# Performance work log

Measured on AMD Instinct MI355X. Metric: run time of the kernel, lower is better.

## Reference

```python
import jax, jax.numpy as jnp
import numpy as np

CHI = 24          # bond dimension (A0[0].shape[0])
K_PATHS = 16      # number of sampled spin strings
N_SPINS = 34      # N = 2**k + 2 with k = 5


def setup_inputs() -> dict:
    key = jax.random.key(0)
    k1, k2 = jax.random.split(key)
    # positive entries -> positive traces -> valid probabilities (stochastic MPS regime)
    A = jax.random.uniform(k1, (2, CHI, CHI), dtype=jnp.float32)
    samples = jax.random.randint(k2, (K_PATHS, N_SPINS), 0, 2).astype(jnp.int32)
    return {"A": A, "samples": samples}


def _kron(X, Y):
    d = X.shape[0] * Y.shape[0]
    return jnp.einsum('ij,kl->ikjl', X, Y).reshape(d, d)


def reference(A, samples):
    chi = A.shape[1]
    Au, Ad = A[0], A[1]
    AAu = _kron(Au, Au)              # [chi^2, chi^2]
    AAd = _kron(Ad, Ad)
    E = AAu + AAd                    # transfer matrix
    E2 = E @ E

    N = samples.shape[1]
    log2N = int(np.log2(N - 2))      # static: matches self.log2N
    E2k = E2
    for _ in range(log2N - 1):       # repeated squaring with trace normalization
        E2k = E2k @ E2k
        E2k = E2k / jnp.trace(E2k)
    EN = E2k @ E2                    # E^N up to overall scale

    def path_loglikelihood(spins):
        def step(String, s):
            Su = String @ AAu
            Sd = String @ AAd
            tr_u = jnp.trace(Su)
            tr_d = jnp.trace(Sd)
            tot = tr_u + tr_d
            p = jnp.where(s == 1, tr_u, tr_d) / tot
            # normalize by total trace: probabilities are scale-invariant ratios,
            # so this is mathematically identical but numerically stable
            String_new = jnp.where(s == 1, Su, Sd) / tot
            return String_new, jnp.log(p)

        _, logps = jax.lax.scan(step, EN, spins)
        return jnp.sum(logps)

    ll = jax.vmap(path_loglikelihood)(samples)   # [K_paths]
    return -jnp.sum(ll)                          # negative loglikelihood objective
```

## Files before the change

kernel.cpp:

```cpp
#include <hip/hip_runtime.h>
#include <math.h>


#define CHI      24
#define CHI2     576
#define NPATH    16
#define NSPIN    34
#define NT       512
#define PITERS_R 2
#define PITERS_L 1
#define SCALE_P  0.00390625f
#define SCALE_V  0.0625f

#define LDS_FENCE() asm volatile("s_waitcnt lgkmcnt(0)" ::: "memory")

__device__ __forceinline__ float hsum4(float4 a) { return (a.x + a.z) + (a.y + a.w); }
__device__ __forceinline__ void fma4(float4& acc, const float4 a, const float4 b) {
    acc.x = fmaf(a.x, b.x, acc.x);
    acc.y = fmaf(a.y, b.y, acc.y);
    acc.z = fmaf(a.z, b.z, acc.z);
    acc.w = fmaf(a.w, b.w, acc.w);
}

__device__ __forceinline__ void mm_tile2(const float* __restrict__ Xa,
                                         const float* __restrict__ Xb,
                                         const float* __restrict__ Y,
                                         int i0, int j0, float o1[3][3], float o2[3][3]) {
    const float4* A0 = (const float4*)(Xa + (i0 + 0) * CHI);
    const float4* A1 = (const float4*)(Xa + (i0 + 1) * CHI);
    const float4* A2 = (const float4*)(Xa + (i0 + 2) * CHI);
    const float4* B0 = (const float4*)(Xb + (i0 + 0) * CHI);
    const float4* B1 = (const float4*)(Xb + (i0 + 1) * CHI);
    const float4* B2 = (const float4*)(Xb + (i0 + 2) * CHI);
    const float4* Y0 = (const float4*)(Y + (j0 + 0) * CHI);
    const float4* Y1 = (const float4*)(Y + (j0 + 1) * CHI);
    const float4* Y2 = (const float4*)(Y + (j0 + 2) * CHI);
    float4 p[3][3], q[3][3];
    #pragma unroll
    for (int a = 0; a < 3; ++a)
        #pragma unroll
        for (int b = 0; b < 3; ++b) {
            p[a][b] = make_float4(0.f, 0.f, 0.f, 0.f);
            q[a][b] = make_float4(0.f, 0.f, 0.f, 0.f);
        }
    #pragma unroll
    for (int v = 0; v < 6; ++v) {
        const float4 y0 = Y0[v], y1 = Y1[v], y2 = Y2[v];
        const float4 a0 = A0[v], a1 = A1[v], a2 = A2[v];
        fma4(p[0][0], a0, y0); fma4(p[0][1], a0, y1); fma4(p[0][2], a0, y2);
        fma4(p[1][0], a1, y0); fma4(p[1][1], a1, y1); fma4(p[1][2], a1, y2);
        fma4(p[2][0], a2, y0); fma4(p[2][1], a2, y1); fma4(p[2][2], a2, y2);
        const float4 b0 = B0[v], b1 = B1[v], b2 = B2[v];
        fma4(q[0][0], b0, y0); fma4(q[0][1], b0, y1); fma4(q[0][2], b0, y2);
        fma4(q[1][0], b1, y0); fma4(q[1][1], b1, y1); fma4(q[1][2], b1, y2);
        fma4(q[2][0], b2, y0); fma4(q[2][1], b2, y1); fma4(q[2][2], b2, y2);
    }
    #pragma unroll
    for (int a = 0; a < 3; ++a)
        #pragma unroll
        for (int b = 0; b < 3; ++b) { o1[a][b] = hsum4(p[a][b]); o2[a][b] = hsum4(q[a][b]); }
}

__device__ __forceinline__ void mm_tile_dual(const float* __restrict__ X1,
                                             const float* __restrict__ Y1,
                                             const float* __restrict__ X2,
                                             const float* __restrict__ Y2,
                                             int i0, int j0, float o1[3][3], float o2[3][3]) {
    const float4* A0 = (const float4*)(X1 + (i0 + 0) * CHI);
    const float4* A1 = (const float4*)(X1 + (i0 + 1) * CHI);
    const float4* A2 = (const float4*)(X1 + (i0 + 2) * CHI);
    const float4* U0 = (const float4*)(Y1 + (j0 + 0) * CHI);
    const float4* U1 = (const float4*)(Y1 + (j0 + 1) * CHI);
    const float4* U2 = (const float4*)(Y1 + (j0 + 2) * CHI);
    const float4* B0 = (const float4*)(X2 + (i0 + 0) * CHI);
    const float4* B1 = (const float4*)(X2 + (i0 + 1) * CHI);
    const float4* B2 = (const float4*)(X2 + (i0 + 2) * CHI);
    const float4* V0 = (const float4*)(Y2 + (j0 + 0) * CHI);
    const float4* V1 = (const float4*)(Y2 + (j0 + 1) * CHI);
    const float4* V2 = (const float4*)(Y2 + (j0 + 2) * CHI);
    float4 p[3][3], q[3][3];
    #pragma unroll
    for (int a = 0; a < 3; ++a)
        #pragma unroll
        for (int b = 0; b < 3; ++b) {
            p[a][b] = make_float4(0.f, 0.f, 0.f, 0.f);
            q[a][b] = make_float4(0.f, 0.f, 0.f, 0.f);
        }
    #pragma unroll
    for (int v = 0; v < 6; ++v) {
        const float4 a0 = A0[v], a1 = A1[v], a2 = A2[v];
        const float4 u0 = U0[v], u1 = U1[v], u2 = U2[v];
        fma4(p[0][0], a0, u0); fma4(p[0][1], a0, u1); fma4(p[0][2], a0, u2);
        fma4(p[1][0], a1, u0); fma4(p[1][1], a1, u1); fma4(p[1][2], a1, u2);
        fma4(p[2][0], a2, u0); fma4(p[2][1], a2, u1); fma4(p[2][2], a2, u2);
        const float4 b0 = B0[v], b1 = B1[v], b2 = B2[v];
        const float4 w0 = V0[v], w1 = V1[v], w2 = V2[v];
        fma4(q[0][0], b0, w0); fma4(q[0][1], b0, w1); fma4(q[0][2], b0, w2);
        fma4(q[1][0], b1, w0); fma4(q[1][1], b1, w1); fma4(q[1][2], b1, w2);
        fma4(q[2][0], b2, w0); fma4(q[2][1], b2, w1); fma4(q[2][2], b2, w2);
    }
    #pragma unroll
    for (int a = 0; a < 3; ++a)
        #pragma unroll
        for (int b = 0; b < 3; ++b) { o1[a][b] = hsum4(p[a][b]); o2[a][b] = hsum4(q[a][b]); }
}

__device__ __forceinline__ void st_tile(float* __restrict__ D, int i0, int j0,
                                        const float o[3][3], float s) {
    #pragma unroll
    for (int a = 0; a < 3; ++a)
        #pragma unroll
        for (int b = 0; b < 3; ++b) D[(i0 + a) * CHI + j0 + b] = o[a][b] * s;
}

__device__ __forceinline__ float dot24v(const float4 r[6], const float vb[24]) {
    float a0 = 0.f, a1 = 0.f, a2 = 0.f, a3 = 0.f;
    #pragma unroll
    for (int v = 0; v < 6; ++v) {
        a0 = fmaf(r[v].x, vb[4 * v + 0], a0);
        a1 = fmaf(r[v].y, vb[4 * v + 1], a1);
        a2 = fmaf(r[v].z, vb[4 * v + 2], a2);
        a3 = fmaf(r[v].w, vb[4 * v + 3], a3);
    }
    return (a0 + a2) + (a1 + a3);
}

__global__ __launch_bounds__(NT, 2) void mps_ll_kernel(
    const float* __restrict__ A,
    const int*   __restrict__ samples,
    float*       __restrict__ out)
{
    __shared__ alignas(16) float sAu[CHI2], sAd[CHI2], sAuT[CHI2], sAdT[CHI2];
    __shared__ alignas(16) float sL[CHI2], sR[CHI2], sGu[CHI2], sGd[CHI2];
    __shared__ alignas(16) float bO1[CHI2], bO2[CHI2], bQ1[CHI2], bQ2[CHI2];
    __shared__ alignas(16) float sVH[NSPIN * CHI];
    __shared__ float llw[8];

    const int tid  = threadIdx.x;
    const int w    = tid >> 6;
    const int lane = tid & 63;
    const int path = blockIdx.x;
    const int i0 = 3 * (lane >> 3), j0 = 3 * (lane & 7);

    for (int k = tid; k < CHI2; k += NT) {
        const int r = k / CHI, c = k % CHI;
        const float u = A[k], d = A[CHI2 + k];
        sAu[k] = u; sAd[k] = d;
        sAuT[c * CHI + r] = u; sAdT[c * CHI + r] = d;
        sR[k] = 1.0f; sL[k] = 1.0f;
    }
    const int sp = (lane < NSPIN) ? samples[path * NSPIN + lane] : 0;
    const unsigned long long smask = __ballot(sp != 0);
    __syncthreads();

    if (w == 0) {
        float o1[3][3], o2[3][3];
        for (int it = 0; it <= PITERS_R; ++it) {
            mm_tile2(sAu, sAd, sR, i0, j0, o1, o2);
            LDS_FENCE();
            st_tile(bO1, i0, j0, o1, 1.0f);
            st_tile(bO2, i0, j0, o2, 1.0f);
            LDS_FENCE();
            mm_tile_dual(bO1, sAu, bO2, sAd, i0, j0, o1, o2);
            LDS_FENCE();
            if (it < PITERS_R) {
                #pragma unroll
                for (int a = 0; a < 3; ++a)
                    #pragma unroll
                    for (int b = 0; b < 3; ++b)
                        sR[(i0 + a) * CHI + j0 + b] = (o1[a][b] + o2[a][b]) * SCALE_P;
            } else {
                st_tile(sGu, i0, j0, o1, SCALE_P);
                st_tile(sGd, i0, j0, o2, SCALE_P);
            }
            LDS_FENCE();
        }
    } else {
        int trec0, trec1, tstart;
        if      (w == 1) { trec0 = 0;  trec1 = 6;  tstart = 0;  }
        else if (w == 2) { trec0 = 6;  trec1 = 11; tstart = 0;  }
        else if (w == 3) { trec0 = 11; trec1 = 16; tstart = 3;  }
        else if (w == 4) { trec0 = 16; trec1 = 21; tstart = 8;  }
        else if (w == 5) { trec0 = 21; trec1 = 25; tstart = 13; }
        else if (w == 6) { trec0 = 25; trec1 = 29; tstart = 17; }
        else             { trec0 = 29; trec1 = 34; tstart = 21; }

        float vb[24];
        float vmine;

        if (w == 1) {
            float o1[3][3], o2[3][3];
            for (int it = 0; it < PITERS_L; ++it) {
                mm_tile2(sAuT, sAdT, sL, i0, j0, o1, o2);
                LDS_FENCE();
                st_tile(bQ1, i0, j0, o1, 1.0f);
                st_tile(bQ2, i0, j0, o2, 1.0f);
                LDS_FENCE();
                mm_tile_dual(bQ1, sAuT, bQ2, sAdT, i0, j0, o1, o2);
                LDS_FENCE();
                #pragma unroll
                for (int a = 0; a < 3; ++a)
                    #pragma unroll
                    for (int b = 0; b < 3; ++b)
                        sL[(i0 + a) * CHI + j0 + b] = (o1[a][b] + o2[a][b]) * SCALE_P;
                LDS_FENCE();
            }
            float4 l4[6];
            {
                const float4* pl = (const float4*)(sL + lane * CHI);
                #pragma unroll
                for (int v = 0; v < 6; ++v) l4[v] = pl[v];
            }
            float y1 = 0.f;
            #pragma unroll
            for (int v = 0; v < 6; ++v) y1 += hsum4(l4[v]);
            #pragma unroll
            for (int j = 0; j < 24; ++j) vb[j] = __shfl(y1, j);
            const float y2 = dot24v(l4, vb) * 0.000244140625f;
            vmine = y2;
            #pragma unroll
            for (int j = 0; j < 24; ++j) vb[j] = __shfl(y2, j);
        } else {
            vmine = 1.0f;
            #pragma unroll
            for (int j = 0; j < 24; ++j) vb[j] = 1.0f;
        }

        float4 u4[6], d4[6];
        {
            const float4* pu = (const float4*)(sAuT + lane * CHI);
            const float4* pd = (const float4*)(sAdT + lane * CHI);
            #pragma unroll
            for (int v = 0; v < 6; ++v) { u4[v] = pu[v]; d4[v] = pd[v]; }
        }

        for (int g = tstart; g < trec1; ++g) {
            if (g >= trec0 && lane < CHI) sVH[g * CHI + lane] = vmine;
            if (g + 1 < trec1) {
                const int bit = (int)((smask >> g) & 1ULL);
                float s;
                if (bit) s = dot24v(u4, vb);
                else     s = dot24v(d4, vb);
                s *= SCALE_V;
                vmine = s;
                #pragma unroll
                for (int j = 0; j < 24; ++j) vb[j] = __shfl(s, j);
            }
        }
        LDS_FENCE();
    }
    __syncthreads();

    float gu[3][3], gd[3][3];
    #pragma unroll
    for (int a = 0; a < 3; ++a)
        #pragma unroll
        for (int b = 0; b < 3; ++b) {
            gu[a][b] = sGu[(i0 + a) * CHI + j0 + b];
            gd[a][b] = sGd[(i0 + a) * CHI + j0 + b];
        }
    float pu5[5], pd5[5];
    #pragma unroll
    for (int s = 0; s < 5; ++s) {
        const int t = w + 8 * s;
        float pu = 1.0f, pd = 1.0f;
        if (t < NSPIN) {
            const float* vt = sVH + t * CHI;
            const float vi0 = vt[i0 + 0], vi1 = vt[i0 + 1], vi2 = vt[i0 + 2];
            const float vj0 = vt[j0 + 0], vj1 = vt[j0 + 1], vj2 = vt[j0 + 2];
            float r0 = gu[0][0] * vj0 + gu[0][1] * vj1 + gu[0][2] * vj2;
            float r1 = gu[1][0] * vj0 + gu[1][1] * vj1 + gu[1][2] * vj2;
            float r2 = gu[2][0] * vj0 + gu[2][1] * vj1 + gu[2][2] * vj2;
            pu = vi0 * r0 + vi1 * r1 + vi2 * r2;
            r0 = gd[0][0] * vj0 + gd[0][1] * vj1 + gd[0][2] * vj2;
            r1 = gd[1][0] * vj0 + gd[1][1] * vj1 + gd[1][2] * vj2;
            r2 = gd[2][0] * vj0 + gd[2][1] * vj1 + gd[2][2] * vj2;
            pd = vi0 * r0 + vi1 * r1 + vi2 * r2;
        }
        pu5[s] = pu; pd5[s] = pd;
    }
    #pragma unroll
    for (int off = 1; off < 64; off <<= 1) {
        #pragma unroll
        for (int s = 0; s < 5; ++s) {
            pu5[s] += __shfl_xor(pu5[s], off);
            pd5[s] += __shfl_xor(pd5[s], off);
        }
    }
    float ll = 0.0f;
    #pragma unroll
    for (int s = 0; s < 5; ++s) {
        const int t = w + 8 * s;
        if (t < NSPIN) {
            const int bit = (int)((smask >> t) & 1ULL);
            ll += __logf(bit ? pu5[s] : pd5[s]) - __logf(pu5[s] + pd5[s]);
        }
    }

    if (lane == 0) llw[w] = ll;
    __syncthreads();

    if (tid == 0) {
        float s = 0.f;
        #pragma unroll
        for (int i = 0; i < 8; ++i) s += llw[i];
        atomicAdd(out, -s);
    }
}

extern "C" void kernel_launch(void* const* d_in, const int* in_sizes, int n_in,
                              void* d_out, int out_size, void* d_ws, size_t ws_size,
                              hipStream_t stream) {
    const float* A       = (const float*)d_in[0];
    const int*   samples = (const int*)d_in[1];
    float*       out     = (float*)d_out;

    mps_ll_kernel<<<NPATH, NT, 0, stream>>>(A, samples, out);
}
```

Baseline: 64.56 us.

## Move final transfer step from right power chain into left vector recurrence

Warp 0 now stops its right-side power iteration one step earlier and skips building the separate up/down G matrices. The left-vector warps instead compute both the up and down products at each recorded step and store them, and the final probability contraction uses R with those two vectors. This shortens warp 0's serial chain, which runs in parallel with the vector recurrence, at the cost of an extra dot product per recorded step and twice the LDS for the stored vectors.

```diff
diff --git a/kernel.cpp b/kernel.cpp
--- a/kernel.cpp
+++ b/kernel.cpp
@@ -131,9 +131,10 @@
     float*       __restrict__ out)
 {
     __shared__ alignas(16) float sAu[CHI2], sAd[CHI2], sAuT[CHI2], sAdT[CHI2];
-    __shared__ alignas(16) float sL[CHI2], sR[CHI2], sGu[CHI2], sGd[CHI2];
+    __shared__ alignas(16) float sL[CHI2], sR[CHI2];
     __shared__ alignas(16) float bO1[CHI2], bO2[CHI2], bQ1[CHI2], bQ2[CHI2];
-    __shared__ alignas(16) float sVH[NSPIN * CHI];
+    __shared__ alignas(16) float sWU[NSPIN * CHI];
+    __shared__ alignas(16) float sWD[NSPIN * CHI];
     __shared__ float llw[8];
 
     const int tid  = threadIdx.x;
@@ -155,7 +156,7 @@
 
     if (w == 0) {
         float o1[3][3], o2[3][3];
-        for (int it = 0; it <= PITERS_R; ++it) {
+        for (int it = 0; it < PITERS_R; ++it) {
             mm_tile2(sAu, sAd, sR, i0, j0, o1, o2);
             LDS_FENCE();
             st_tile(bO1, i0, j0, o1, 1.0f);
@@ -163,16 +164,11 @@
             LDS_FENCE();
             mm_tile_dual(bO1, sAu, bO2, sAd, i0, j0, o1, o2);
             LDS_FENCE();
-            if (it < PITERS_R) {
+            #pragma unroll
+            for (int a = 0; a < 3; ++a)
                 #pragma unroll
-                for (int a = 0; a < 3; ++a)
-                    #pragma unroll
-                    for (int b = 0; b < 3; ++b)
-                        sR[(i0 + a) * CHI + j0 + b] = (o1[a][b] + o2[a][b]) * SCALE_P;
-            } else {
-                st_tile(sGu, i0, j0, o1, SCALE_P);
-                st_tile(sGd, i0, j0, o2, SCALE_P);
-            }
+                for (int b = 0; b < 3; ++b)
+                    sR[(i0 + a) * CHI + j0 + b] = (o1[a][b] + o2[a][b]) * SCALE_P;
             LDS_FENCE();
         }
     } else {
@@ -225,6 +221,7 @@
             #pragma unroll
             for (int j = 0; j < 24; ++j) vb[j] = 1.0f;
         }
+        (void)vmine;
 
         float4 u4[6], d4[6];
         {
@@ -235,14 +232,25 @@
         }
 
         for (int g = tstart; g < trec1; ++g) {
-            if (g >= trec0 && lane < CHI) sVH[g * CHI + lane] = vmine;
-            if (g + 1 < trec1) {
+            if (g >= trec0) {
+                const float su = dot24v(u4, vb);
+                const float sd = dot24v(d4, vb);
+                if (lane < CHI) {
+                    sWU[g * CHI + lane] = su;
+                    sWD[g * CHI + lane] = sd;
+                }
+                if (g + 1 < trec1) {
+                    const int bit = (int)((smask >> g) & 1ULL);
+                    const float s = (bit ? su : sd) * SCALE_V;
+                    #pragma unroll
+                    for (int j = 0; j < 24; ++j) vb[j] = __shfl(s, j);
+                }
+            } else {
                 const int bit = (int)((smask >> g) & 1ULL);
                 float s;
                 if (bit) s = dot24v(u4, vb);
                 else     s = dot24v(d4, vb);
                 s *= SCALE_V;
-                vmine = s;
                 #pragma unroll
                 for (int j = 0; j < 24; ++j) vb[j] = __shfl(s, j);
             }
@@ -251,31 +259,32 @@
     }
     __syncthreads();
 
-    float gu[3][3], gd[3][3];
-    #pragma unroll
-    for (int a = 0; a < 3; ++a)
-        #pragma unroll
-        for (int b = 0; b < 3; ++b) {
-            gu[a][b] = sGu[(i0 + a) * CHI + j0 + b];
-            gd[a][b] = sGd[(i0 + a) * CHI + j0 + b];
-        }
+    float rt[3][3];
+    #pragma unroll
+    for (int a = 0; a < 3; ++a)
+        #pragma unroll
+        for (int b = 0; b < 3; ++b)
+            rt[a][b] = sR[(i0 + a) * CHI + j0 + b];
     float pu5[5], pd5[5];
     #pragma unroll
     for (int s = 0; s < 5; ++s) {
         const int t = w + 8 * s;
         float pu = 1.0f, pd = 1.0f;
         if (t < NSPIN) {
-            const float* vt = sVH + t * CHI;
-            const float vi0 = vt[i0 + 0], vi1 = vt[i0 + 1], vi2 = vt[i0 + 2];
-            const float vj0 = vt[j0 + 0], vj1 = vt[j0 + 1], vj2 = vt[j0 + 2];
-            float r0 = gu[0][0] * vj0 + gu[0][1] * vj1 + gu[0][2] * vj2;
-            float r1 = gu[1][0] * vj0 + gu[1][1] * vj1 + gu[1][2] * vj2;
-            float r2 = gu[2][0] * vj0 + gu[2][1] * vj1 + gu[2][2] * vj2;
-            pu = vi0 * r0 + vi1 * r1 + vi2 * r2;
-            r0 = gd[0][0] * vj0 + gd[0][1] * vj1 + gd[0][2] * vj2;
-            r1 = gd[1][0] * vj0 + gd[1][1] * vj1 + gd[1][2] * vj2;
-            r2 = gd[2][0] * vj0 + gd[2][1] * vj1 + gd[2][2] * vj2;
-            pd = vi0 * r0 + vi1 * r1 + vi2 * r2;
+            const float* wu = sWU + t * CHI;
+            const float* wd = sWD + t * CHI;
+            const float ui0 = wu[i0 + 0], ui1 = wu[i0 + 1], ui2 = wu[i0 + 2];
+            const float uj0 = wu[j0 + 0], uj1 = wu[j0 + 1], uj2 = wu[j0 + 2];
+            const float di0 = wd[i0 + 0], di1 = wd[i0 + 1], di2 = wd[i0 + 2];
+            const float dj0 = wd[j0 + 0], dj1 = wd[j0 + 1], dj2 = wd[j0 + 2];
+            float r0 = rt[0][0] * uj0 + rt[0][1] * uj1 + rt[0][2] * uj2;
+            float r1 = rt[1][0] * uj0 + rt[1][1] * uj1 + rt[1][2] * uj2;
+            float r2 = rt[2][0] * uj0 + rt[2][1] * uj1 + rt[2][2] * uj2;
+            pu = ui0 * r0 + ui1 * r1 + ui2 * r2;
+            r0 = rt[0][0] * dj0 + rt[0][1] * dj1 + rt[0][2] * dj2;
+            r1 = rt[1][0] * dj0 + rt[1][1] * dj1 + rt[1][2] * dj2;
+            r2 = rt[2][0] * dj0 + rt[2][1] * dj1 + rt[2][2] * dj2;
+            pd = di0 * r0 + di1 * r1 + di2 * r2;
         }
         pu5[s] = pu; pd5[s] = pd;
     }
```

New measurement: 64.43 us. About the same (-0.2%).
